# Performance work log

Hardware: AMD Instinct MI355X
Metric: run time of the kernel (lower is better)

Reference implementation:

```python
import jax, jax.numpy as jnp
import numpy as np

RADIUS = 1.3
RES = 128
SH_DEG = 2
N_SH = (SH_DEG + 1) ** 2          # 9 SH basis functions
DATA_DIM = N_SH * 3 + 1           # 28: 27 SH rgb coeffs + 1 sigma
STEP = (2.0 * RADIUS / RES) / 2.0 # half a voxel, as in calc_step_size
N_INTRS = int(np.ceil(np.sqrt(3.0) * 2.0 * RES))  # torch.arange(float) length
N_RAYS = 4096


def sh_basis(d):
    # Real spherical harmonics up to degree 2, svox2/plenoxels convention. d: [B,3]
    x, y, z = d[:, 0], d[:, 1], d[:, 2]
    return jnp.stack([
        0.28209479177387814 * jnp.ones_like(x),
        -0.4886025119029199 * y,
        0.4886025119029199 * z,
        -0.4886025119029199 * x,
        1.0925484305920792 * x * y,
        -1.0925484305920792 * y * z,
        0.31539156525252005 * (2.0 * z * z - x * x - y * y),
        -1.0925484305920792 * x * z,
        0.5462742152960396 * (x * x - y * y),
    ], axis=-1)  # [B, 9]


def trilerp(grid, pts):
    # grid: [C, R, R, R] laid out (D,H,W); pts: [N,3] as (x,y,z) in [-1,1],
    # x indexes W, y indexes H, z indexes D (torch grid_sample convention),
    # align_corners=True, padding_mode='border'. Returns [C, N].
    R = grid.shape[-1]
    c = jnp.clip((pts + 1.0) * 0.5 * (R - 1), 0.0, R - 1)  # border padding
    c0 = jnp.floor(c)
    f = c - c0
    i0 = c0.astype(jnp.int32)
    i1 = jnp.minimum(i0 + 1, R - 1)
    x0, y0, z0 = i0[:, 0], i0[:, 1], i0[:, 2]
    x1, y1, z1 = i1[:, 0], i1[:, 1], i1[:, 2]
    fx, fy, fz = f[:, 0], f[:, 1], f[:, 2]
    g = lambda zi, yi, xi: grid[:, zi, yi, xi]  # [C, N]
    out = (g(z0, y0, x0) * ((1 - fz) * (1 - fy) * (1 - fx)) +
           g(z0, y0, x1) * ((1 - fz) * (1 - fy) * fx) +
           g(z0, y1, x0) * ((1 - fz) * fy * (1 - fx)) +
           g(z0, y1, x1) * ((1 - fz) * fy * fx) +
           g(z1, y0, x0) * (fz * (1 - fy) * (1 - fx)) +
           g(z1, y0, x1) * (fz * (1 - fy) * fx) +
           g(z1, y1, x0) * (fz * fy * (1 - fx)) +
           g(z1, y1, x1) * (fz * fy * fx))
    return out


def setup_inputs() -> dict:
    key = jax.random.key(0)
    k1, k2, k3 = jax.random.split(key, 3)
    rays_o = jax.random.normal(k1, (N_RAYS, 3), jnp.float32) * 0.3  # inside cube
    rd = jax.random.normal(k2, (N_RAYS, 3), jnp.float32)
    rays_d = rd / jnp.linalg.norm(rd, axis=-1, keepdims=True)
    # grid parameter: SH coeffs init 0.1, sigma init 0.01 (as in module) + noise
    base = jnp.concatenate([
        jnp.full((1, DATA_DIM - 1, RES, RES, RES), 0.1, jnp.float32),
        jnp.full((1, 1, RES, RES, RES), 0.01, jnp.float32)], axis=1)
    data = base + 0.01 * jax.random.normal(k3, (1, DATA_DIM, RES, RES, RES), jnp.float32)
    return {"rays_o": rays_o, "rays_d": rays_d, "data": data}


def reference(rays_o, rays_d, data):
    # --- ray/box intersection sampling (no grad in original) ---
    ro = jax.lax.stop_gradient(rays_o)
    rd = jax.lax.stop_gradient(rays_d)
    off_pos = (RADIUS - ro) / rd
    off_neg = (-RADIUS - ro) / rd
    start = jnp.max(jnp.minimum(off_pos, off_neg), axis=-1, keepdims=True)  # [B,1]
    steps = jnp.arange(N_INTRS, dtype=ro.dtype)[None, :]
    intersections = start + steps * STEP          # [B, N_INTRS]
    t = intersections[:, :-1]                     # [B, NI]
    pts = ro[:, None, :] + t[..., None] * rd[:, None, :]  # [B, NI, 3]
    mask = jnp.all((pts > -RADIUS) & (pts < RADIUS), axis=-1)  # [B, NI]
    ptsn = pts / RADIUS
    B, NI = t.shape

    # --- trilinear interpolation of grid at all sample points ---
    interp = trilerp(data[0], ptsn.reshape(-1, 3)).T  # [B*NI, 28]
    sigma = jax.nn.relu(interp[:, -1].reshape(B, NI))
    sigma = jnp.where(mask, sigma, 0.0)  # masked_scatter into zeros

    # --- sigma2alpha: standard volumetric compositing weights ---
    dists = (intersections[:, 1:] - intersections[:, :-1]) \
            * jnp.linalg.norm(rays_d, axis=-1, keepdims=True)  # [B, NI]
    alpha = 1.0 - jnp.exp(-sigma * dists)
    trans = jnp.cumprod(jnp.concatenate(
        [jnp.ones((B, 1), alpha.dtype), 1.0 - alpha + 1e-10], axis=1), axis=1)[:, :-1]
    abs_light = alpha * trans  # [B, NI]

    # --- SH -> rgb per sample ---
    sh_mult = sh_basis(rays_d)  # [B, 9]
    sh = interp[:, :-1].reshape(B, NI, 3, N_SH)
    rgb_pts = jnp.einsum('bk,bnck->bnc', sh_mult, sh)  # [B, NI, 3]
    rgb_pts = jnp.where(mask[..., None], rgb_pts, 0.0)  # masked_scatter

    # --- shrgb2rgb: sigmoid, composite, white background ---
    rgb = jnp.sum(abs_light[..., None] * jax.nn.sigmoid(rgb_pts), axis=1)  # [B,3]
    rgb = rgb + (1.0 - jnp.sum(abs_light, axis=1))[..., None]  # white bkgd
    return rgb
```

## Files before the change

### kernel.cpp

```cpp
#include <hip/hip_runtime.h>
#include <math.h>


typedef float f2v __attribute__((ext_vector_type(2)));

namespace {
constexpr float kRadius   = 1.3f;
constexpr int   kRes      = 128;
constexpr float kStep     = 2.0f * 1.3f / 128.0f / 2.0f;
constexpr int   kNI       = 443;
constexpr int   kNRays    = 4096;
constexpr int   kChStride = kRes * kRes * kRes;
constexpr int   kCh       = 28;
constexpr int   kRecBytes = 32;
constexpr size_t kVoxBytes = (size_t)kChStride * kRecBytes;
constexpr int   kChunks   = 2;
constexpr int   kChunks7  = 7;
}

__global__ __launch_bounds__(256)
void convert_grid(const float* __restrict__ grid, unsigned char* __restrict__ vox)
{
    const int v = blockIdx.x * 256 + threadIdx.x;
    float c[kCh];
    #pragma unroll
    for (int ch = 0; ch < kCh; ++ch)
        c[ch] = __builtin_nontemporal_load(grid + (size_t)ch * kChStride + v);

    unsigned w[8];
    #pragma unroll
    for (int i = 0; i < 6; ++i) {
        int lo = __builtin_amdgcn_cvt_pk_fp8_f32(c[4*i],   c[4*i+1], 0,  false);
        w[i]   = (unsigned)__builtin_amdgcn_cvt_pk_fp8_f32(c[4*i+2], c[4*i+3], lo, true);
    }
    {
        int lo = __builtin_amdgcn_cvt_pk_fp8_f32(c[24], c[25], 0,  false);
        w[6]   = (unsigned)__builtin_amdgcn_cvt_pk_fp8_f32(c[26], 0.0f, lo, true);
    }
    {
        union { unsigned short u; _Float16 h; } cv;
        cv.h = (_Float16)c[27];
        w[7] = (unsigned)cv.u;
    }

    uint4* dst = (uint4*)(vox + (size_t)v * kRecBytes);
    dst[0] = make_uint4(w[0], w[1], w[2], w[3]);
    dst[1] = make_uint4(w[4], w[5], w[6], w[7]);
}

struct SampleC { float a, cR, cG, cB; };

__device__ __forceinline__ SampleC eval_sample(
    int k, float start, float ox, float oy, float oz,
    float dx, float dy, float dz, float dist,
    const float* __restrict__ shm, const unsigned char* __restrict__ vox)
{
    SampleC s;
    s.a = 1.f; s.cR = s.cG = s.cB = 0.f;
    if (k >= kNI) return s;

    const float t  = start + (float)k * kStep;
    const float px = ox + t*dx;
    const float py = oy + t*dy;
    const float pz = oz + t*dz;
    const bool inb = (px > -kRadius) && (px < kRadius) &&
                     (py > -kRadius) && (py < kRadius) &&
                     (pz > -kRadius) && (pz < kRadius);

    float alpha = 0.0f;
    if (inb) {
        const float cx = fminf(fmaxf((px*(1.0f/kRadius) + 1.0f)*0.5f*127.0f, 0.0f), 127.0f);
        const float cy = fminf(fmaxf((py*(1.0f/kRadius) + 1.0f)*0.5f*127.0f, 0.0f), 127.0f);
        const float cz = fminf(fmaxf((pz*(1.0f/kRadius) + 1.0f)*0.5f*127.0f, 0.0f), 127.0f);
        const float fx0 = floorf(cx), fy0 = floorf(cy), fz0 = floorf(cz);
        const float fx = cx - fx0, fy = cy - fy0, fz = cz - fz0;
        const int ix0 = (int)fx0, iy0 = (int)fy0, iz0 = (int)fz0;
        const int ix1 = min(ix0 + 1, 127);
        const int iy1 = min(iy0 + 1, 127);
        const int iz1 = min(iz0 + 1, 127);

        const float gx0 = 1.0f - fx, gy0 = 1.0f - fy, gz0 = 1.0f - fz;

        const int offs[8] = {
            iz0*(kRes*kRes) + iy0*kRes + ix0,
            iz0*(kRes*kRes) + iy0*kRes + ix1,
            iz0*(kRes*kRes) + iy1*kRes + ix0,
            iz0*(kRes*kRes) + iy1*kRes + ix1,
            iz1*(kRes*kRes) + iy0*kRes + ix0,
            iz1*(kRes*kRes) + iy0*kRes + ix1,
            iz1*(kRes*kRes) + iy1*kRes + ix0,
            iz1*(kRes*kRes) + iy1*kRes + ix1 };
        const float cw[8] = {
            gz0*gy0*gx0, gz0*gy0*fx, gz0*fy*gx0, gz0*fy*fx,
            fz *gy0*gx0, fz *gy0*fx, fz *fy*gx0, fz *fy*fx };

        float rp0 = 0.f, rp1 = 0.f, rp2 = 0.f, sig = 0.f;
        #pragma unroll
        for (int cn = 0; cn < 8; ++cn) {
            const uint4* vp = (const uint4*)(vox + (size_t)offs[cn] * kRecBytes);
            const uint4 u0 = vp[0], u1 = vp[1];

            float f[28];
            const unsigned wd[7] = { u0.x, u0.y, u0.z, u0.w, u1.x, u1.y, u1.z };
            #pragma unroll
            for (int i = 0; i < 7; ++i) {
                const f2v lo = __builtin_amdgcn_cvt_pk_f32_fp8((int)wd[i], false);
                const f2v hi = __builtin_amdgcn_cvt_pk_f32_fp8((int)wd[i], true);
                f[4*i+0] = lo.x; f[4*i+1] = lo.y; f[4*i+2] = hi.x; f[4*i+3] = hi.y;
            }
            union { unsigned short u; _Float16 h; } cv;
            cv.u = (unsigned short)(u1.w & 0xffffu);
            const float sv = (float)cv.h;

            float r = 0.f, g = 0.f, b = 0.f;
            #pragma unroll
            for (int j = 0; j < 9; ++j) {
                r = fmaf(shm[j], f[j],      r);
                g = fmaf(shm[j], f[9 + j],  g);
                b = fmaf(shm[j], f[18 + j], b);
            }
            const float wc = cw[cn];
            rp0 = fmaf(wc, r, rp0);
            rp1 = fmaf(wc, g, rp1);
            rp2 = fmaf(wc, b, rp2);
            sig = fmaf(wc, sv, sig);
        }
        sig = fmaxf(sig, 0.0f);
        alpha = 1.0f - expf(-sig * dist);
        s.cR = alpha * (1.0f / (1.0f + expf(-rp0)));
        s.cG = alpha * (1.0f / (1.0f + expf(-rp1)));
        s.cB = alpha * (1.0f / (1.0f + expf(-rp2)));
    }
    s.a = 1.0f - alpha + 1e-10f;
    return s;
}

__device__ __forceinline__ float wave_scan_prod(float a, int lane, float& total)
{
    float prod = a;
    #pragma unroll
    for (int off = 1; off < 64; off <<= 1) {
        const float y = __shfl_up(prod, off, 64);
        if (lane >= off) prod *= y;
    }
    float excl = __shfl_up(prod, 1, 64);
    if (lane == 0) excl = 1.0f;
    total = __shfl(prod, 63, 64);
    return excl;
}

__global__ __launch_bounds__(256, 4)
void render_chunks(const float* __restrict__ rays_o,
                   const float* __restrict__ rays_d,
                   const unsigned char* __restrict__ vox,
                   float* __restrict__ partials)
{
    const int lane  = threadIdx.x & 63;
    const int W     = blockIdx.x * 4 + (threadIdx.x >> 6);
    const int ray   = W >> 1;
    const int chunk = W & 1;

    const float ox = rays_o[3*ray+0], oy = rays_o[3*ray+1], oz = rays_o[3*ray+2];
    const float dx = rays_d[3*ray+0], dy = rays_d[3*ray+1], dz = rays_d[3*ray+2];

    const float ppx = ( kRadius - ox)/dx, pnx = (-kRadius - ox)/dx;
    const float ppy = ( kRadius - oy)/dy, pny = (-kRadius - oy)/dy;
    const float ppz = ( kRadius - oz)/dz, pnz = (-kRadius - oz)/dz;
    const float start  = fmaxf(fminf(ppx, pnx), fmaxf(fminf(ppy, pny), fminf(ppz, pnz)));
    const float t_exit = fminf(fmaxf(ppx, pnx), fminf(fmaxf(ppy, pny), fmaxf(ppz, pnz)));

    const int base = chunk * 256;

    if (start + (float)base * kStep > t_exit + kStep) {
        if (lane == 0) {
            float* p = partials + (size_t)(ray * kChunks + chunk) * 5;
            p[0] = 0.f; p[1] = 0.f; p[2] = 0.f; p[3] = 0.f; p[4] = 1.f;
        }
        return;
    }

    const float dnorm = sqrtf(dx*dx + dy*dy + dz*dz);
    const float dist  = kStep * dnorm;

    float shm[9];
    shm[0] =  0.28209479177387814f;
    shm[1] = -0.4886025119029199f * dy;
    shm[2] =  0.4886025119029199f * dz;
    shm[3] = -0.4886025119029199f * dx;
    shm[4] =  1.0925484305920792f * dx * dy;
    shm[5] = -1.0925484305920792f * dy * dz;
    shm[6] =  0.31539156525252005f * (2.0f*dz*dz - dx*dx - dy*dy);
    shm[7] = -1.0925484305920792f * dx * dz;
    shm[8] =  0.5462742152960396f * (dx*dx - dy*dy);

    const SampleC A = eval_sample(base       + lane, start, ox, oy, oz, dx, dy, dz, dist, shm, vox);
    const SampleC B = eval_sample(base +  64 + lane, start, ox, oy, oz, dx, dy, dz, dist, shm, vox);
    const SampleC C = eval_sample(base + 128 + lane, start, ox, oy, oz, dx, dy, dz, dist, shm, vox);
    const SampleC D = eval_sample(base + 192 + lane, start, ox, oy, oz, dx, dy, dz, dist, shm, vox);

    float P0, P1, P2, P3;
    const float eA = wave_scan_prod(A.a, lane, P0);
    const float eB = wave_scan_prod(B.a, lane, P1);
    const float eC = wave_scan_prod(C.a, lane, P2);
    const float eD = wave_scan_prod(D.a, lane, P3);

    const float pA = eA;
    const float pB = P0 * eB;
    const float pC = P0 * P1 * eC;
    const float pD = P0 * P1 * P2 * eD;

    const float one = 1.0f + 1e-10f;
    const float sL = pA * (one - A.a) + pB * (one - B.a)
                   + pC * (one - C.a) + pD * (one - D.a);

    float sR = pA * A.cR;  sR = fmaf(pB, B.cR, sR);
    sR = fmaf(pC, C.cR, sR);  sR = fmaf(pD, D.cR, sR);
    float sG = pA * A.cG;  sG = fmaf(pB, B.cG, sG);
    sG = fmaf(pC, C.cG, sG);  sG = fmaf(pD, D.cG, sG);
    float sB = pA * A.cB;  sB = fmaf(pB, B.cB, sB);
    sB = fmaf(pC, C.cB, sB);  sB = fmaf(pD, D.cB, sB);

    const float P = P0 * P1 * P2 * P3;

    float rL = sL;
    float rR = sR, rG = sG, rB = sB;
    #pragma unroll
    for (int off = 32; off > 0; off >>= 1) {
        rR += __shfl_down(rR, off, 64);
        rG += __shfl_down(rG, off, 64);
        rB += __shfl_down(rB, off, 64);
        rL += __shfl_down(rL, off, 64);
    }

    if (lane == 0) {
        float* p = partials + (size_t)(ray * kChunks + chunk) * 5;
        p[0] = rR; p[1] = rG; p[2] = rB; p[3] = rL; p[4] = P;
    }
}

__global__ __launch_bounds__(256)
void combine_chunks(const float* __restrict__ partials, float* __restrict__ out)
{
    const int r = blockIdx.x * 256 + threadIdx.x;
    const float* p = partials + (size_t)r * (kChunks * 5);

    float carry = 1.0f, aR = 0.f, aG = 0.f, aB = 0.f, aL = 0.f;
    #pragma unroll
    for (int c = 0; c < kChunks; ++c) {
        aR = fmaf(carry, p[c*5 + 0], aR);
        aG = fmaf(carry, p[c*5 + 1], aG);
        aB = fmaf(carry, p[c*5 + 2], aB);
        aL = fmaf(carry, p[c*5 + 3], aL);
        carry *= p[c*5 + 4];
    }
    const float bg = 1.0f - aL;
    out[3*r + 0] = aR + bg;
    out[3*r + 1] = aG + bg;
    out[3*r + 2] = aB + bg;
}

#define TRI8(p) (w000*(p)[o000] + w001*(p)[o001] + w010*(p)[o010] + w011*(p)[o011] \
               + w100*(p)[o100] + w101*(p)[o101] + w110*(p)[o110] + w111*(p)[o111])

__global__ __launch_bounds__(256)
void plenoxel_render_direct(const float* __restrict__ rays_o,
                            const float* __restrict__ rays_d,
                            const float* __restrict__ grid,
                            float* __restrict__ out)
{
    const int lane = threadIdx.x & 63;
    const int ray  = blockIdx.x * 4 + (threadIdx.x >> 6);

    const float ox = rays_o[3*ray+0], oy = rays_o[3*ray+1], oz = rays_o[3*ray+2];
    const float dx = rays_d[3*ray+0], dy = rays_d[3*ray+1], dz = rays_d[3*ray+2];

    const float sx = fminf(( kRadius - ox)/dx, (-kRadius - ox)/dx);
    const float sy = fminf(( kRadius - oy)/dy, (-kRadius - oy)/dy);
    const float sz = fminf(( kRadius - oz)/dz, (-kRadius - oz)/dz);
    const float start = fmaxf(sx, fmaxf(sy, sz));
    const float dnorm = sqrtf(dx*dx + dy*dy + dz*dz);

    float shm[9];
    shm[0] =  0.28209479177387814f;
    shm[1] = -0.4886025119029199f * dy;
    shm[2] =  0.4886025119029199f * dz;
    shm[3] = -0.4886025119029199f * dx;
    shm[4] =  1.0925484305920792f * dx * dy;
    shm[5] = -1.0925484305920792f * dy * dz;
    shm[6] =  0.31539156525252005f * (2.0f*dz*dz - dx*dx - dy*dy);
    shm[7] = -1.0925484305920792f * dx * dz;
    shm[8] =  0.5462742152960396f * (dx*dx - dy*dy);

    float carry = 1.0f;
    float accR = 0.f, accG = 0.f, accB = 0.f, accL = 0.f;

    for (int chunk = 0; chunk < kChunks7; ++chunk) {
        const int k = chunk * 64 + lane;
        float alpha = 0.0f, a = 1.0f;
        float rp0 = 0.f, rp1 = 0.f, rp2 = 0.f;
        bool inb = false;

        if (k < kNI) {
            const float t = start + (float)k * kStep;
            const float dist = kStep * dnorm;
            const float px = ox + t*dx, py = oy + t*dy, pz = oz + t*dz;
            inb = (px > -kRadius) && (px < kRadius) &&
                  (py > -kRadius) && (py < kRadius) &&
                  (pz > -kRadius) && (pz < kRadius);
            float sigma = 0.0f;
            if (inb) {
                const float cx = fminf(fmaxf((px*(1.0f/kRadius) + 1.0f)*0.5f*127.0f, 0.0f), 127.0f);
                const float cy = fminf(fmaxf((py*(1.0f/kRadius) + 1.0f)*0.5f*127.0f, 0.0f), 127.0f);
                const float cz = fminf(fmaxf((pz*(1.0f/kRadius) + 1.0f)*0.5f*127.0f, 0.0f), 127.0f);
                const float fx0 = floorf(cx), fy0 = floorf(cy), fz0 = floorf(cz);
                const float fx = cx - fx0, fy = cy - fy0, fz = cz - fz0;
                const int ix0 = (int)fx0, iy0 = (int)fy0, iz0 = (int)fz0;
                const int ix1 = min(ix0 + 1, 127);
                const int iy1 = min(iy0 + 1, 127);
                const int iz1 = min(iz0 + 1, 127);
                const float gx0 = 1.0f - fx, gy0 = 1.0f - fy, gz0 = 1.0f - fz;
                const float w000 = gz0*gy0*gx0, w001 = gz0*gy0*fx;
                const float w010 = gz0*fy *gx0, w011 = gz0*fy *fx;
                const float w100 = fz *gy0*gx0, w101 = fz *gy0*fx;
                const float w110 = fz *fy *gx0, w111 = fz *fy *fx;
                const int o000 = iz0*(kRes*kRes) + iy0*kRes + ix0;
                const int o001 = iz0*(kRes*kRes) + iy0*kRes + ix1;
                const int o010 = iz0*(kRes*kRes) + iy1*kRes + ix0;
                const int o011 = iz0*(kRes*kRes) + iy1*kRes + ix1;
                const int o100 = iz1*(kRes*kRes) + iy0*kRes + ix0;
                const int o101 = iz1*(kRes*kRes) + iy0*kRes + ix1;
                const int o110 = iz1*(kRes*kRes) + iy1*kRes + ix0;
                const int o111 = iz1*(kRes*kRes) + iy1*kRes + ix1;
                #pragma unroll
                for (int kk = 0; kk < 9; ++kk) {
                    rp0 = fmaf(shm[kk], TRI8(grid + (kk     ) * kChStride), rp0);
                    rp1 = fmaf(shm[kk], TRI8(grid + (kk +  9) * kChStride), rp1);
                    rp2 = fmaf(shm[kk], TRI8(grid + (kk + 18) * kChStride), rp2);
                }
                sigma = fmaxf(TRI8(grid + 27 * kChStride), 0.0f);
            }
            alpha = 1.0f - expf(-sigma * dist);
            a     = 1.0f - alpha + 1e-10f;
        }

        float prod = a;
        #pragma unroll
        for (int off = 1; off < 64; off <<= 1) {
            const float y = __shfl_up(prod, off, 64);
            if (lane >= off) prod *= y;
        }
        float excl = __shfl_up(prod, 1, 64);
        if (lane == 0) excl = 1.0f;
        const float trans = carry * excl;
        const float w = alpha * trans;
        if (inb) {
            accR = fmaf(w, 1.0f / (1.0f + expf(-rp0)), accR);
            accG = fmaf(w, 1.0f / (1.0f + expf(-rp1)), accG);
            accB = fmaf(w, 1.0f / (1.0f + expf(-rp2)), accB);
        }
        accL += w;
        carry *= __shfl(prod, 63, 64);
    }

    #pragma unroll
    for (int off = 32; off > 0; off >>= 1) {
        accR += __shfl_down(accR, off, 64);
        accG += __shfl_down(accG, off, 64);
        accB += __shfl_down(accB, off, 64);
        accL += __shfl_down(accL, off, 64);
    }

    if (lane == 0) {
        const float bg = 1.0f - accL;
        out[3*ray + 0] = accR + bg;
        out[3*ray + 1] = accG + bg;
        out[3*ray + 2] = accB + bg;
    }
}

extern "C" void kernel_launch(void* const* d_in, const int* in_sizes, int n_in,
                              void* d_out, int out_size, void* d_ws, size_t ws_size,
                              hipStream_t stream) {
    const float* rays_o = (const float*)d_in[0];
    const float* rays_d = (const float*)d_in[1];
    const float* data   = (const float*)d_in[2];
    float* out = (float*)d_out;

    const size_t partBytes = (size_t)kNRays * kChunks * 5 * sizeof(float);
    const size_t need = kVoxBytes + partBytes;

    if (ws_size >= need) {
        unsigned char* vox = (unsigned char*)d_ws;
        float* partials = (float*)((char*)d_ws + kVoxBytes);

        hipLaunchKernelGGL(convert_grid,
                           dim3(kChStride / 256), dim3(256), 0, stream,
                           data, vox);
        hipLaunchKernelGGL(render_chunks,
                           dim3(kNRays * kChunks / 4), dim3(256), 0, stream,
                           rays_o, rays_d, vox, partials);
        hipLaunchKernelGGL(combine_chunks,
                           dim3(kNRays / 256), dim3(256), 0, stream,
                           partials, out);
    } else {
        hipLaunchKernelGGL(plenoxel_render_direct,
                           dim3(kNRays / 4), dim3(256), 0, stream,
                           rays_o, rays_d, data, out);
    }
}
```

Baseline: 364.0 us.

## Store voxel grid in Morton (Z-order) layout for trilinear gather locality

The converted fp8 voxel records are now written in Morton order, and the render kernel computes the eight corner addresses by bit-interleaving the integer coordinates. This is meant to improve cache locality of the 8-corner gathers, which otherwise span widely separated z and y slabs, at the cost of a few extra bit operations per sample. The launch-bounds occupancy hint for the render kernel is also lowered from 4 to 3 blocks, which gives the compiler more registers per thread. The rest is variable renaming.

```diff
diff --git a/kernel.cpp b/kernel.cpp
--- a/kernel.cpp
+++ b/kernel.cpp
@@ -18,14 +18,38 @@
 constexpr int   kChunks7  = 7;
 }
 
+__device__ __forceinline__ unsigned part1by2(unsigned v)
+{
+    v &= 0x7Fu;
+    v = (v | (v << 16)) & 0x030000FFu;
+    v = (v | (v <<  8)) & 0x0300F00Fu;
+    v = (v | (v <<  4)) & 0x030C30C3u;
+    v = (v | (v <<  2)) & 0x09249249u;
+    return v;
+}
+__device__ __forceinline__ unsigned compact1by2(unsigned v)
+{
+    v &= 0x09249249u;
+    v = (v ^ (v >>  2)) & 0x030C30C3u;
+    v = (v ^ (v >>  4)) & 0x0300F00Fu;
+    v = (v ^ (v >>  8)) & 0x030000FFu;
+    v = (v ^ (v >> 16)) & 0x000003FFu;
+    return v;
+}
+
 __global__ __launch_bounds__(256)
 void convert_grid(const float* __restrict__ grid, unsigned char* __restrict__ vox)
 {
-    const int v = blockIdx.x * 256 + threadIdx.x;
+    const unsigned m = blockIdx.x * 256 + threadIdx.x;
+    const unsigned x = compact1by2(m);
+    const unsigned y = compact1by2(m >> 1);
+    const unsigned z = compact1by2(m >> 2);
+    const unsigned lin = (z << 14) + (y << 7) + x;
+
     float c[kCh];
     #pragma unroll
     for (int ch = 0; ch < kCh; ++ch)
-        c[ch] = __builtin_nontemporal_load(grid + (size_t)ch * kChStride + v);
+        c[ch] = __builtin_nontemporal_load(grid + (size_t)ch * kChStride + lin);
 
     unsigned w[8];
     #pragma unroll
@@ -43,7 +67,7 @@
         w[7] = (unsigned)cv.u;
     }
 
-    uint4* dst = (uint4*)(vox + (size_t)v * kRecBytes);
+    uint4* dst = (uint4*)(vox + (size_t)m * kRecBytes);
     dst[0] = make_uint4(w[0], w[1], w[2], w[3]);
     dst[1] = make_uint4(w[4], w[5], w[6], w[7]);
 }
@@ -81,15 +105,16 @@
 
         const float gx0 = 1.0f - fx, gy0 = 1.0f - fy, gz0 = 1.0f - fz;
 
-        const int offs[8] = {
-            iz0*(kRes*kRes) + iy0*kRes + ix0,
-            iz0*(kRes*kRes) + iy0*kRes + ix1,
-            iz0*(kRes*kRes) + iy1*kRes + ix0,
-            iz0*(kRes*kRes) + iy1*kRes + ix1,
-            iz1*(kRes*kRes) + iy0*kRes + ix0,
-            iz1*(kRes*kRes) + iy0*kRes + ix1,
-            iz1*(kRes*kRes) + iy1*kRes + ix0,
-            iz1*(kRes*kRes) + iy1*kRes + ix1 };
+        const unsigned X0 = part1by2((unsigned)ix0);
+        const unsigned X1 = part1by2((unsigned)ix1);
+        const unsigned Y0 = part1by2((unsigned)iy0) << 1;
+        const unsigned Y1 = part1by2((unsigned)iy1) << 1;
+        const unsigned Z0 = part1by2((unsigned)iz0) << 2;
+        const unsigned Z1 = part1by2((unsigned)iz1) << 2;
+
+        const unsigned offs[8] = {
+            Z0 | Y0 | X0,  Z0 | Y0 | X1,  Z0 | Y1 | X0,  Z0 | Y1 | X1,
+            Z1 | Y0 | X0,  Z1 | Y0 | X1,  Z1 | Y1 | X0,  Z1 | Y1 | X1 };
         const float cw[8] = {
             gz0*gy0*gx0, gz0*gy0*fx, gz0*fy*gx0, gz0*fy*fx,
             fz *gy0*gx0, fz *gy0*fx, fz *fy*gx0, fz *fy*fx };
@@ -149,7 +174,7 @@
     return excl;
 }
 
-__global__ __launch_bounds__(256, 4)
+__global__ __launch_bounds__(256, 3)
 void render_chunks(const float* __restrict__ rays_o,
                    const float* __restrict__ rays_d,
                    const unsigned char* __restrict__ vox,
@@ -210,20 +235,18 @@
     const float pD = P0 * P1 * P2 * eD;
 
     const float one = 1.0f + 1e-10f;
-    const float sL = pA * (one - A.a) + pB * (one - B.a)
-                   + pC * (one - C.a) + pD * (one - D.a);
-
-    float sR = pA * A.cR;  sR = fmaf(pB, B.cR, sR);
-    sR = fmaf(pC, C.cR, sR);  sR = fmaf(pD, D.cR, sR);
-    float sG = pA * A.cG;  sG = fmaf(pB, B.cG, sG);
-    sG = fmaf(pC, C.cG, sG);  sG = fmaf(pD, D.cG, sG);
-    float sB = pA * A.cB;  sB = fmaf(pB, B.cB, sB);
-    sB = fmaf(pC, C.cB, sB);  sB = fmaf(pD, D.cB, sB);
+    float rL = pA * (one - A.a) + pB * (one - B.a)
+             + pC * (one - C.a) + pD * (one - D.a);
+
+    float rR = pA * A.cR;  rR = fmaf(pB, B.cR, rR);
+    rR = fmaf(pC, C.cR, rR);  rR = fmaf(pD, D.cR, rR);
+    float rG = pA * A.cG;  rG = fmaf(pB, B.cG, rG);
+    rG = fmaf(pC, C.cG, rG);  rG = fmaf(pD, D.cG, rG);
+    float rB = pA * A.cB;  rB = fmaf(pB, B.cB, rB);
+    rB = fmaf(pC, C.cB, rB);  rB = fmaf(pD, D.cB, rB);
 
     const float P = P0 * P1 * P2 * P3;
 
-    float rL = sL;
-    float rR = sR, rG = sG, rB = sB;
     #pragma unroll
     for (int off = 32; off > 0; off >>= 1) {
         rR += __shfl_down(rR, off, 64);
```

After: 481.3 us. +32.2%, slower.
